# Optimization experiments

Hardware: AMD Instinct MI355X
Metric: run time of the kernel (lower is better)

Reference implementation:

```python
import jax, jax.numpy as jnp
import numpy as np

B, T, C, H = 4, 2048, 1024, 16
D = C // H  # head_dim = 64


def setup_inputs() -> dict:
    key = jax.random.key(0)
    k1, k2, k3 = jax.random.split(key, 3)
    x = jax.random.normal(k1, (B, T, C), dtype=jnp.float32)
    w_attn = jax.random.normal(k2, (C, 3 * C), dtype=jnp.float32) * (1.0 / np.sqrt(C))
    b_attn = jnp.zeros((3 * C,), dtype=jnp.float32)
    w_proj = jax.random.normal(k3, (C, C), dtype=jnp.float32) * (1.0 / np.sqrt(C))
    b_proj = jnp.zeros((C,), dtype=jnp.float32)
    return {"x": x, "w_attn": w_attn, "b_attn": b_attn, "w_proj": w_proj, "b_proj": b_proj}


def reference(x, w_attn, b_attn, w_proj, b_proj):
    Bx, Tx, Cx = x.shape
    qkv = x @ w_attn + b_attn                      # (B, T, 3C)
    q, k, v = jnp.split(qkv, 3, axis=2)
    # (B, T, C) -> (B, H, T, D)
    q = q.reshape(Bx, Tx, H, D).transpose(0, 2, 1, 3)
    k = k.reshape(Bx, Tx, H, D).transpose(0, 2, 1, 3)
    v = v.reshape(Bx, Tx, H, D).transpose(0, 2, 1, 3)
    scores = jnp.einsum('bhqd,bhkd->bhqk', q, k) / jnp.sqrt(jnp.float32(D))
    causal = jnp.tril(jnp.ones((Tx, Tx), dtype=bool))
    scores = jnp.where(causal[None, None], scores, jnp.float32(-jnp.inf))
    probs = jax.nn.softmax(scores, axis=-1)
    out = jnp.einsum('bhqk,bhkd->bhqd', probs, v)  # (B, H, T, D)
    out = out.transpose(0, 2, 1, 3).reshape(Bx, Tx, Cx)
    return out @ w_proj + b_proj
```

## Files before the change

kernel.cpp:

```cpp
#include <hip/hip_runtime.h>

#define AS1 __attribute__((address_space(1)))
#define AS3 __attribute__((address_space(3)))

using bf16x8  = __attribute__((ext_vector_type(8))) __bf16;
using floatx4 = __attribute__((ext_vector_type(4))) float;

#define SCQ 0.18033688f

__device__ inline ushort f2b(float f) {
    __bf16 h = (__bf16)f;
    return __builtin_bit_cast(ushort, h);
}

__global__ void k_conv(const float* __restrict__ in, ushort* __restrict__ out, int n) {
    int i = (blockIdx.x * 256 + threadIdx.x) * 4;
    if (i < n) {
        float4 v = *(const float4*)(in + i);
        ushort4 o;
        o.x = f2b(v.x); o.y = f2b(v.y); o.z = f2b(v.z); o.w = f2b(v.w);
        *(ushort4*)(out + i) = o;
    }
}

__global__ void k_transpose(const float* __restrict__ in, ushort* __restrict__ out,
                            int R, int Ncol, float scale, int scale_cols) {
    __shared__ float tile[32][33];
    int tx = threadIdx.x & 31, ty = threadIdx.x >> 5;
    int c0 = blockIdx.x * 32, r0 = blockIdx.y * 32;
    for (int i = 0; i < 32; i += 8)
        tile[ty + i][tx] = in[(size_t)(r0 + ty + i) * Ncol + c0 + tx];
    __syncthreads();
    for (int i = 0; i < 32; i += 8) {
        int n = c0 + ty + i;
        float v = tile[tx][ty + i];
        if (n < scale_cols) v *= scale;
        out[(size_t)n * R + r0 + tx] = f2b(v);
    }
}

__global__ __launch_bounds__(256, 2) void k_gemm_bt(
    const ushort* __restrict__ A, const ushort* __restrict__ Bt,
    const float* __restrict__ bias, float* __restrict__ outv,
    int M, int N, int K)
{
    __shared__ __align__(16) ushort As[128 * 32];
    __shared__ __align__(16) ushort Bs[128 * 32];
    int tid = threadIdx.x;
    int m0 = blockIdx.y * 128, n0 = blockIdx.x * 128;
    int lane = tid & 63;
    int wm = (tid >> 7) * 64;
    int wn = ((tid >> 6) & 1) * 64;
    int lr = lane & 15, quad = lane >> 4, lk = quad * 8;

    floatx4 acc[4][4] = {};
    const ushort* ag = A  + (size_t)(m0 + (tid >> 2)) * K + (tid & 3) * 8;
    const ushort* bg = Bt + (size_t)(n0 + (tid >> 2)) * K + (tid & 3) * 8;
    ushort* asd = &As[tid * 8];
    ushort* bsd = &Bs[tid * 8];

    for (int kt = 0; kt < K; kt += 32) {
        __builtin_amdgcn_global_load_lds((const AS1 unsigned int*)(ag + kt),                  (AS3 unsigned int*)(asd),        16, 0, 0);
        __builtin_amdgcn_global_load_lds((const AS1 unsigned int*)(ag + kt + (size_t)64 * K), (AS3 unsigned int*)(asd + 2048), 16, 0, 0);
        __builtin_amdgcn_global_load_lds((const AS1 unsigned int*)(bg + kt),                  (AS3 unsigned int*)(bsd),        16, 0, 0);
        __builtin_amdgcn_global_load_lds((const AS1 unsigned int*)(bg + kt + (size_t)64 * K), (AS3 unsigned int*)(bsd + 2048), 16, 0, 0);
        asm volatile("s_waitcnt vmcnt(0)" ::: "memory");
        __syncthreads();
        bf16x8 af[4], bf[4];
        #pragma unroll
        for (int i = 0; i < 4; ++i) af[i] = *(const bf16x8*)&As[(wm + 16 * i + lr) * 32 + lk];
        #pragma unroll
        for (int j = 0; j < 4; ++j) bf[j] = *(const bf16x8*)&Bs[(wn + 16 * j + lr) * 32 + lk];
        #pragma unroll
        for (int i = 0; i < 4; ++i)
            #pragma unroll
            for (int j = 0; j < 4; ++j)
                acc[i][j] = __builtin_amdgcn_mfma_f32_16x16x32_bf16(af[i], bf[j], acc[i][j], 0, 0, 0);
        __syncthreads();
    }

    #pragma unroll
    for (int j = 0; j < 4; ++j) {
        int col = n0 + wn + 16 * j + lr;
        float bv = bias[col];
        #pragma unroll
        for (int i = 0; i < 4; ++i) {
            int row = m0 + wm + 16 * i + quad * 4;
            #pragma unroll
            for (int r = 0; r < 4; ++r)
                outv[(size_t)(row + r) * N + col] = acc[i][j][r] + bv;
        }
    }
}

__global__ __launch_bounds__(256, 2) void k_gemm_qkv(
    const ushort* __restrict__ A, const ushort* __restrict__ Bt,
    const float* __restrict__ bias, ushort* __restrict__ qkv, ushort* __restrict__ vt)
{
    constexpr int K = 1024;
    __shared__ __align__(16) ushort As[128 * 32];
    __shared__ __align__(16) ushort Bs[128 * 32];
    int tid = threadIdx.x;
    int m0 = blockIdx.y * 128, n0 = blockIdx.x * 128;
    int lane = tid & 63;
    int wm = (tid >> 7) * 64;
    int wn = ((tid >> 6) & 1) * 64;
    int lr = lane & 15, quad = lane >> 4, lk = quad * 8;

    floatx4 acc[4][4] = {};
    const ushort* ag = A  + (size_t)(m0 + (tid >> 2)) * K + (tid & 3) * 8;
    const ushort* bg = Bt + (size_t)(n0 + (tid >> 2)) * K + (tid & 3) * 8;
    ushort* asd = &As[tid * 8];
    ushort* bsd = &Bs[tid * 8];

    for (int kt = 0; kt < K; kt += 32) {
        __builtin_amdgcn_global_load_lds((const AS1 unsigned int*)(ag + kt),                  (AS3 unsigned int*)(asd),        16, 0, 0);
        __builtin_amdgcn_global_load_lds((const AS1 unsigned int*)(ag + kt + (size_t)64 * K), (AS3 unsigned int*)(asd + 2048), 16, 0, 0);
        __builtin_amdgcn_global_load_lds((const AS1 unsigned int*)(bg + kt),                  (AS3 unsigned int*)(bsd),        16, 0, 0);
        __builtin_amdgcn_global_load_lds((const AS1 unsigned int*)(bg + kt + (size_t)64 * K), (AS3 unsigned int*)(bsd + 2048), 16, 0, 0);
        asm volatile("s_waitcnt vmcnt(0)" ::: "memory");
        __syncthreads();
        bf16x8 af[4], bf[4];
        #pragma unroll
        for (int i = 0; i < 4; ++i) af[i] = *(const bf16x8*)&As[(wm + 16 * i + lr) * 32 + lk];
        #pragma unroll
        for (int j = 0; j < 4; ++j) bf[j] = *(const bf16x8*)&Bs[(wn + 16 * j + lr) * 32 + lk];
        #pragma unroll
        for (int i = 0; i < 4; ++i)
            #pragma unroll
            for (int j = 0; j < 4; ++j)
                acc[i][j] = __builtin_amdgcn_mfma_f32_16x16x32_bf16(af[i], bf[j], acc[i][j], 0, 0, 0);
        __syncthreads();
    }

    int bb = m0 >> 11;
    #pragma unroll
    for (int j = 0; j < 4; ++j) {
        int col = n0 + wn + 16 * j + lr;
        float bv = bias[col];
        if (col < 1024) bv *= SCQ;
        if (col < 2048) {
            #pragma unroll
            for (int i = 0; i < 4; ++i) {
                int row = m0 + wm + 16 * i + quad * 4;
                #pragma unroll
                for (int r = 0; r < 4; ++r)
                    qkv[(size_t)(row + r) * 2048 + col] = f2b(acc[i][j][r] + bv);
            }
        } else {
            int h = (col - 2048) >> 6, d = (col - 2048) & 63;
            ushort* vbase = vt + ((size_t)(bb * 16 + h) * 64 + d) * 2048;
            #pragma unroll
            for (int i = 0; i < 4; ++i) {
                int t0 = (m0 + wm + 16 * i + quad * 4) & 2047;
                ushort4 pk;
                ((ushort*)&pk)[0] = f2b(acc[i][j][0] + bv);
                ((ushort*)&pk)[1] = f2b(acc[i][j][1] + bv);
                ((ushort*)&pk)[2] = f2b(acc[i][j][2] + bv);
                ((ushort*)&pk)[3] = f2b(acc[i][j][3] + bv);
                *(ushort4*)&vbase[t0] = pk;
            }
        }
    }
}

__global__ __launch_bounds__(512, 4) void k_attn(const ushort* __restrict__ qkv,
                                                 const ushort* __restrict__ vt,
                                                 ushort* __restrict__ out)
{
    constexpr int T = 2048, SQK = 2048, C = 1024;
    __shared__ __align__(16) ushort Ks[64 * 64];
    __shared__ __align__(16) ushort Vs[64 * 64];
    __shared__ __align__(16) ushort Ps[8 * 16 * 72];
    int tid = threadIdx.x;
    int lane = tid & 63, wave = tid >> 6;
    int lr = lane & 15, quad = lane >> 4, lk = quad * 8;
    int bh = blockIdx.y;
    int b = bh >> 4, h = bh & 15;
    size_t base = (size_t)b * T * SQK;
    const ushort* kg0 = qkv + base + 1024 + h * 64;
    const ushort* vg0 = vt + (size_t)bh * 64 * 2048;
    ushort* psw = &Ps[wave * 16 * 72];

    int srow = tid >> 3;
    int sg   = (tid & 7) ^ (srow & 7);
    ushort* ksdst = &Ks[tid * 8];
    ushort* vsdst = &Vs[tid * 8];
    const ushort* kgs = kg0 + (size_t)srow * SQK + sg * 8;
    const ushort* vgs = vg0 + (size_t)srow * 2048 + sg * 8;

    bf16x8 ones;
    #pragma unroll
    for (int i = 0; i < 8; ++i) ones[i] = (__bf16)1.0f;
    int c0 = (quad ^ (lr & 7)) * 8;
    int c1 = ((4 + quad) ^ (lr & 7)) * 8;

    int qts[2] = { (int)blockIdx.x, 15 - (int)blockIdx.x };
    for (int ti = 0; ti < 2; ++ti) {
        int qt = qts[ti];
        int qrow = qt * 128 + wave * 16;
        int kt_d = qrow >> 6;
        const ushort* qp = qkv + base + (size_t)(qrow + lr) * SQK + h * 64;
        bf16x8 aq0 = *(const bf16x8*)(qp + lk);
        bf16x8 aq1 = *(const bf16x8*)(qp + 32 + lk);
        floatx4 o[4] = {};
        floatx4 lacc = {};
        int ktmax = 2 * qt + 1;

        for (int kt = 0; kt <= ktmax; ++kt) {
            __syncthreads();
            __builtin_amdgcn_global_load_lds((const AS1 unsigned int*)(kgs + (size_t)kt * 64 * SQK),
                                             (AS3 unsigned int*)ksdst, 16, 0, 0);
            __builtin_amdgcn_global_load_lds((const AS1 unsigned int*)(vgs + kt * 64),
                                             (AS3 unsigned int*)vsdst, 16, 0, 0);
            asm volatile("s_waitcnt vmcnt(0)" ::: "memory");
            __syncthreads();
            if (kt > kt_d) continue;

            floatx4 s[4];
            #pragma unroll
            for (int j = 0; j < 4; ++j) {
                const ushort* kr = &Ks[(16 * j + lr) * 64];
                bf16x8 bk0 = *(const bf16x8*)(kr + c0);
                bf16x8 bk1 = *(const bf16x8*)(kr + c1);
                floatx4 z = {};
                s[j] = __builtin_amdgcn_mfma_f32_16x16x32_bf16(aq0, bk0, z, 0, 0, 0);
                s[j] = __builtin_amdgcn_mfma_f32_16x16x32_bf16(aq1, bk1, s[j], 0, 0, 0);
            }
            if (kt == kt_d) {
                int qg = qrow + quad * 4, kb = kt * 64;
                #pragma unroll
                for (int r = 0; r < 4; ++r)
                    #pragma unroll
                    for (int j = 0; j < 4; ++j) {
                        float p = ((kb + 16 * j + lr) > (qg + r)) ? 0.f : exp2f(s[j][r]);
                        psw[(quad * 4 + r) * 72 + 16 * j + lr] = f2b(p);
                    }
            } else {
                #pragma unroll
                for (int r = 0; r < 4; ++r)
                    #pragma unroll
                    for (int j = 0; j < 4; ++j)
                        psw[(quad * 4 + r) * 72 + 16 * j + lr] = f2b(exp2f(s[j][r]));
            }
            asm volatile("s_waitcnt lgkmcnt(0)" ::: "memory");
            bf16x8 ap0 = *(const bf16x8*)&psw[lr * 72 + lk];
            bf16x8 ap1 = *(const bf16x8*)&psw[lr * 72 + 32 + lk];
            lacc = __builtin_amdgcn_mfma_f32_16x16x32_bf16(ap0, ones, lacc, 0, 0, 0);
            lacc = __builtin_amdgcn_mfma_f32_16x16x32_bf16(ap1, ones, lacc, 0, 0, 0);
            #pragma unroll
            for (int jd = 0; jd < 4; ++jd) {
                const ushort* vr = &Vs[(16 * jd + lr) * 64];
                bf16x8 bv0 = *(const bf16x8*)(vr + c0);
                bf16x8 bv1 = *(const bf16x8*)(vr + c1);
                o[jd] = __builtin_amdgcn_mfma_f32_16x16x32_bf16(ap0, bv0, o[jd], 0, 0, 0);
                o[jd] = __builtin_amdgcn_mfma_f32_16x16x32_bf16(ap1, bv1, o[jd], 0, 0, 0);
            }
        }

        #pragma unroll
        for (int r = 0; r < 4; ++r) {
            float inv = 1.0f / lacc[r];
            int row = b * T + qrow + quad * 4 + r;
            #pragma unroll
            for (int jd = 0; jd < 4; ++jd)
                out[(size_t)row * C + h * 64 + 16 * jd + lr] = f2b(o[jd][r] * inv);
        }
    }
}

extern "C" void kernel_launch(void* const* d_in, const int* in_sizes, int n_in,
                              void* d_out, int out_size, void* d_ws, size_t ws_size,
                              hipStream_t stream) {
    const float* x      = (const float*)d_in[0];
    const float* w_attn = (const float*)d_in[1];
    const float* b_attn = (const float*)d_in[2];
    const float* w_proj = (const float*)d_in[3];
    const float* b_proj = (const float*)d_in[4];
    float* out = (float*)d_out;

    constexpr int Bb = 4, T = 2048, C = 1024;
    constexpr int M = Bb * T;

    ushort* xb  = (ushort*)d_ws;
    ushort* waT = xb  + (size_t)M * C;
    ushort* wpT = waT + (size_t)3 * C * C;
    ushort* qkv = wpT + (size_t)C * C;
    ushort* vt  = qkv + (size_t)M * 2 * C;
    ushort* ao  = vt  + (size_t)64 * 64 * T;

    k_conv<<<(M * C / 4 + 255) / 256, 256, 0, stream>>>(x, xb, M * C);
    k_transpose<<<dim3(3 * C / 32, C / 32), 256, 0, stream>>>(w_attn, waT, C, 3 * C, SCQ, C);
    k_transpose<<<dim3(C / 32, C / 32), 256, 0, stream>>>(w_proj, wpT, C, C, 1.0f, 0);
    k_gemm_qkv<<<dim3(3 * C / 128, M / 128), 256, 0, stream>>>(xb, waT, b_attn, qkv, vt);
    k_attn<<<dim3(8, Bb * 16), 512, 0, stream>>>(qkv, vt, ao);
    k_gemm_bt<<<dim3(C / 128, M / 128), 256, 0, stream>>>(ao, wpT, b_proj, out, M, C, C);
}
```

Before: 262.5 us.

## Restructure attention to 128-key tiles with 32 query rows per wave

The attention kernel moves from 512 threads handling 16 query rows per wave over 64-key tiles to 256 threads handling 32 query rows per wave over 128-key tiles. S is computed transposed (K as the A operand) so each lane writes packed 4-wide P values, and each V fragment is reused across two query subtiles. The aim is to halve the number of K/V loads and barriers per query block, raise MFMA reuse per LDS read, and drop the idle iterations of the old loop. The cost is more registers, more shared memory per block and fewer waves per block.

```diff
diff --git a/kernel.cpp b/kernel.cpp
--- a/kernel.cpp
+++ b/kernel.cpp
@@ -164,108 +164,138 @@
     }
 }
 
-__global__ __launch_bounds__(512, 4) void k_attn(const ushort* __restrict__ qkv,
+__global__ __launch_bounds__(256, 2) void k_attn(const ushort* __restrict__ qkv,
                                                  const ushort* __restrict__ vt,
                                                  ushort* __restrict__ out)
 {
     constexpr int T = 2048, SQK = 2048, C = 1024;
-    __shared__ __align__(16) ushort Ks[64 * 64];
-    __shared__ __align__(16) ushort Vs[64 * 64];
-    __shared__ __align__(16) ushort Ps[8 * 16 * 72];
+    constexpr int PSTR = 136;
+    __shared__ __align__(16) ushort Ks[128 * 64];
+    __shared__ __align__(16) ushort Vs[64 * 128];
+    __shared__ __align__(16) ushort Ps[4 * 32 * PSTR];
     int tid = threadIdx.x;
     int lane = tid & 63, wave = tid >> 6;
-    int lr = lane & 15, quad = lane >> 4, lk = quad * 8;
+    int lr = lane & 15, quad = lane >> 4;
     int bh = blockIdx.y;
     int b = bh >> 4, h = bh & 15;
     size_t base = (size_t)b * T * SQK;
     const ushort* kg0 = qkv + base + 1024 + h * 64;
     const ushort* vg0 = vt + (size_t)bh * 64 * 2048;
-    ushort* psw = &Ps[wave * 16 * 72];
-
-    int srow = tid >> 3;
-    int sg   = (tid & 7) ^ (srow & 7);
-    ushort* ksdst = &Ks[tid * 8];
-    ushort* vsdst = &Vs[tid * 8];
-    const ushort* kgs = kg0 + (size_t)srow * SQK + sg * 8;
-    const ushort* vgs = vg0 + (size_t)srow * 2048 + sg * 8;
+    ushort* psw = &Ps[wave * 32 * PSTR];
 
     bf16x8 ones;
     #pragma unroll
     for (int i = 0; i < 8; ++i) ones[i] = (__bf16)1.0f;
-    int c0 = (quad ^ (lr & 7)) * 8;
-    int c1 = ((4 + quad) ^ (lr & 7)) * 8;
+
+    int kslot[4], vslot[4];
+    #pragma unroll
+    for (int it = 0; it < 4; ++it) { kslot[it] = tid + 256 * it; vslot[it] = tid + 256 * it; }
 
     int qts[2] = { (int)blockIdx.x, 15 - (int)blockIdx.x };
     for (int ti = 0; ti < 2; ++ti) {
         int qt = qts[ti];
-        int qrow = qt * 128 + wave * 16;
-        int kt_d = qrow >> 6;
-        const ushort* qp = qkv + base + (size_t)(qrow + lr) * SQK + h * 64;
-        bf16x8 aq0 = *(const bf16x8*)(qp + lk);
-        bf16x8 aq1 = *(const bf16x8*)(qp + 32 + lk);
-        floatx4 o[4] = {};
-        floatx4 lacc = {};
-        int ktmax = 2 * qt + 1;
-
-        for (int kt = 0; kt <= ktmax; ++kt) {
+        int qrowW = qt * 128 + wave * 32;
+        const ushort* qp0 = qkv + base + (size_t)(qrowW + lr) * SQK + h * 64;
+        const ushort* qp1 = qkv + base + (size_t)(qrowW + 16 + lr) * SQK + h * 64;
+        bf16x8 aq00 = *(const bf16x8*)(qp0 + quad * 8);
+        bf16x8 aq01 = *(const bf16x8*)(qp0 + 32 + quad * 8);
+        bf16x8 aq10 = *(const bf16x8*)(qp1 + quad * 8);
+        bf16x8 aq11 = *(const bf16x8*)(qp1 + 32 + quad * 8);
+        floatx4 o[2][4] = {};
+        floatx4 lacc[2] = {};
+
+        for (int kt = 0; kt <= qt; ++kt) {
             __syncthreads();
-            __builtin_amdgcn_global_load_lds((const AS1 unsigned int*)(kgs + (size_t)kt * 64 * SQK),
-                                             (AS3 unsigned int*)ksdst, 16, 0, 0);
-            __builtin_amdgcn_global_load_lds((const AS1 unsigned int*)(vgs + kt * 64),
-                                             (AS3 unsigned int*)vsdst, 16, 0, 0);
+            #pragma unroll
+            for (int it = 0; it < 4; ++it) {
+                int sl = kslot[it];
+                int key = sl >> 3, g = (sl & 7) ^ (key & 7);
+                __builtin_amdgcn_global_load_lds(
+                    (const AS1 unsigned int*)(kg0 + (size_t)(kt * 128 + key) * SQK + g * 8),
+                    (AS3 unsigned int*)&Ks[sl * 8], 16, 0, 0);
+            }
+            #pragma unroll
+            for (int it = 0; it < 4; ++it) {
+                int sl = vslot[it];
+                int dim = sl >> 4, g = (sl & 15) ^ (dim & 15);
+                __builtin_amdgcn_global_load_lds(
+                    (const AS1 unsigned int*)(vg0 + (size_t)dim * 2048 + kt * 128 + g * 8),
+                    (AS3 unsigned int*)&Vs[sl * 8], 16, 0, 0);
+            }
             asm volatile("s_waitcnt vmcnt(0)" ::: "memory");
             __syncthreads();
-            if (kt > kt_d) continue;
-
-            floatx4 s[4];
-            #pragma unroll
-            for (int j = 0; j < 4; ++j) {
-                const ushort* kr = &Ks[(16 * j + lr) * 64];
-                bf16x8 bk0 = *(const bf16x8*)(kr + c0);
-                bf16x8 bk1 = *(const bf16x8*)(kr + c1);
+
+            bool diag = (kt == qt);
+            #pragma unroll
+            for (int jk = 0; jk < 8; ++jk) {
+                const ushort* kr = &Ks[(16 * jk + lr) * 64];
+                bf16x8 ak0 = *(const bf16x8*)(kr + ((quad) ^ (lr & 7)) * 8);
+                bf16x8 ak1 = *(const bf16x8*)(kr + ((4 + quad) ^ (lr & 7)) * 8);
                 floatx4 z = {};
-                s[j] = __builtin_amdgcn_mfma_f32_16x16x32_bf16(aq0, bk0, z, 0, 0, 0);
-                s[j] = __builtin_amdgcn_mfma_f32_16x16x32_bf16(aq1, bk1, s[j], 0, 0, 0);
-            }
-            if (kt == kt_d) {
-                int qg = qrow + quad * 4, kb = kt * 64;
+                floatx4 st0 = __builtin_amdgcn_mfma_f32_16x16x32_bf16(ak0, aq00, z, 0, 0, 0);
+                st0 = __builtin_amdgcn_mfma_f32_16x16x32_bf16(ak1, aq01, st0, 0, 0, 0);
+                floatx4 st1 = __builtin_amdgcn_mfma_f32_16x16x32_bf16(ak0, aq10, z, 0, 0, 0);
+                st1 = __builtin_amdgcn_mfma_f32_16x16x32_bf16(ak1, aq11, st1, 0, 0, 0);
+                int kloc = 16 * jk + quad * 4;
+                if (diag) {
+                    int q0l = wave * 32 + lr;
+                    float p00 = (kloc + 0 > q0l) ? 0.f : exp2f(st0[0]);
+                    float p01 = (kloc + 1 > q0l) ? 0.f : exp2f(st0[1]);
+                    float p02 = (kloc + 2 > q0l) ? 0.f : exp2f(st0[2]);
+                    float p03 = (kloc + 3 > q0l) ? 0.f : exp2f(st0[3]);
+                    int q1l = q0l + 16;
+                    float p10 = (kloc + 0 > q1l) ? 0.f : exp2f(st1[0]);
+                    float p11 = (kloc + 1 > q1l) ? 0.f : exp2f(st1[1]);
+                    float p12 = (kloc + 2 > q1l) ? 0.f : exp2f(st1[2]);
+                    float p13 = (kloc + 3 > q1l) ? 0.f : exp2f(st1[3]);
+                    uint2 w0, w1;
+                    w0.x = (unsigned)f2b(p00) | ((unsigned)f2b(p01) << 16);
+                    w0.y = (unsigned)f2b(p02) | ((unsigned)f2b(p03) << 16);
+                    w1.x = (unsigned)f2b(p10) | ((unsigned)f2b(p11) << 16);
+                    w1.y = (unsigned)f2b(p12) | ((unsigned)f2b(p13) << 16);
+                    *(uint2*)&psw[(lr) * PSTR + kloc]      = w0;
+                    *(uint2*)&psw[(16 + lr) * PSTR + kloc] = w1;
+                } else {
+                    uint2 w0, w1;
+                    w0.x = (unsigned)f2b(exp2f(st0[0])) | ((unsigned)f2b(exp2f(st0[1])) << 16);
+                    w0.y = (unsigned)f2b(exp2f(st0[2])) | ((unsigned)f2b(exp2f(st0[3])) << 16);
+                    w1.x = (unsigned)f2b(exp2f(st1[0])) | ((unsigned)f2b(exp2f(st1[1])) << 16);
+                    w1.y = (unsigned)f2b(exp2f(st1[2])) | ((unsigned)f2b(exp2f(st1[3])) << 16);
+                    *(uint2*)&psw[(lr) * PSTR + kloc]      = w0;
+                    *(uint2*)&psw[(16 + lr) * PSTR + kloc] = w1;
+                }
+            }
+            asm volatile("s_waitcnt lgkmcnt(0)" ::: "memory");
+            bf16x8 ap[2][4];
+            #pragma unroll
+            for (int t = 0; t < 2; ++t)
                 #pragma unroll
-                for (int r = 0; r < 4; ++r)
-                    #pragma unroll
-                    for (int j = 0; j < 4; ++j) {
-                        float p = ((kb + 16 * j + lr) > (qg + r)) ? 0.f : exp2f(s[j][r]);
-                        psw[(quad * 4 + r) * 72 + 16 * j + lr] = f2b(p);
-                    }
-            } else {
+                for (int s = 0; s < 4; ++s) {
+                    ap[t][s] = *(const bf16x8*)&psw[(t * 16 + lr) * PSTR + s * 32 + quad * 8];
+                    lacc[t] = __builtin_amdgcn_mfma_f32_16x16x32_bf16(ap[t][s], ones, lacc[t], 0, 0, 0);
+                }
+            #pragma unroll
+            for (int jd = 0; jd < 4; ++jd) {
+                const ushort* vr = &Vs[(16 * jd + lr) * 128];
                 #pragma unroll
-                for (int r = 0; r < 4; ++r)
-                    #pragma unroll
-                    for (int j = 0; j < 4; ++j)
-                        psw[(quad * 4 + r) * 72 + 16 * j + lr] = f2b(exp2f(s[j][r]));
-            }
-            asm volatile("s_waitcnt lgkmcnt(0)" ::: "memory");
-            bf16x8 ap0 = *(const bf16x8*)&psw[lr * 72 + lk];
-            bf16x8 ap1 = *(const bf16x8*)&psw[lr * 72 + 32 + lk];
-            lacc = __builtin_amdgcn_mfma_f32_16x16x32_bf16(ap0, ones, lacc, 0, 0, 0);
-            lacc = __builtin_amdgcn_mfma_f32_16x16x32_bf16(ap1, ones, lacc, 0, 0, 0);
-            #pragma unroll
-            for (int jd = 0; jd < 4; ++jd) {
-                const ushort* vr = &Vs[(16 * jd + lr) * 64];
-                bf16x8 bv0 = *(const bf16x8*)(vr + c0);
-                bf16x8 bv1 = *(const bf16x8*)(vr + c1);
-                o[jd] = __builtin_amdgcn_mfma_f32_16x16x32_bf16(ap0, bv0, o[jd], 0, 0, 0);
-                o[jd] = __builtin_amdgcn_mfma_f32_16x16x32_bf16(ap1, bv1, o[jd], 0, 0, 0);
+                for (int s = 0; s < 4; ++s) {
+                    bf16x8 bv = *(const bf16x8*)(vr + ((4 * s + quad) ^ lr) * 8);
+                    o[0][jd] = __builtin_amdgcn_mfma_f32_16x16x32_bf16(ap[0][s], bv, o[0][jd], 0, 0, 0);
+                    o[1][jd] = __builtin_amdgcn_mfma_f32_16x16x32_bf16(ap[1][s], bv, o[1][jd], 0, 0, 0);
+                }
             }
         }
 
         #pragma unroll
-        for (int r = 0; r < 4; ++r) {
-            float inv = 1.0f / lacc[r];
-            int row = b * T + qrow + quad * 4 + r;
-            #pragma unroll
-            for (int jd = 0; jd < 4; ++jd)
-                out[(size_t)row * C + h * 64 + 16 * jd + lr] = f2b(o[jd][r] * inv);
-        }
+        for (int t = 0; t < 2; ++t)
+            #pragma unroll
+            for (int r = 0; r < 4; ++r) {
+                float inv = 1.0f / lacc[t][r];
+                int row = b * T + qrowW + t * 16 + quad * 4 + r;
+                #pragma unroll
+                for (int jd = 0; jd < 4; ++jd)
+                    out[(size_t)row * C + h * 64 + 16 * jd + lr] = f2b(o[t][jd][r] * inv);
+            }
     }
 }
 
@@ -293,6 +323,6 @@
     k_transpose<<<dim3(3 * C / 32, C / 32), 256, 0, stream>>>(w_attn, waT, C, 3 * C, SCQ, C);
     k_transpose<<<dim3(C / 32, C / 32), 256, 0, stream>>>(w_proj, wpT, C, C, 1.0f, 0);
     k_gemm_qkv<<<dim3(3 * C / 128, M / 128), 256, 0, stream>>>(xb, waT, b_attn, qkv, vt);
-    k_attn<<<dim3(8, Bb * 16), 512, 0, stream>>>(qkv, vt, ao);
+    k_attn<<<dim3(8, Bb * 16), 256, 0, stream>>>(qkv, vt, ao);
     k_gemm_bt<<<dim3(C / 128, M / 128), 256, 0, stream>>>(ao, wpT, b_proj, out, M, C, C);
 }
```

New measurement: 285.0 us. +8.6%, slower.

## Double-buffer K/V tiles in LDS and compute transposed S for packed P stores

Applied to the files above, without the earlier changes.

The K and V shared-memory tiles are doubled so the next tile's global-to-LDS load is issued right after the barrier and overlaps the current tile's QK^T, softmax and PV work. This replaces the load-then-wait-every-iteration pattern. S is also computed as K·Q^T, so each lane holds four consecutive keys for one query and writes P as a single packed 8-byte store instead of sixteen scalar stores. The cost is twice the LDS for K and V, which may reduce occupancy at 512 threads per block.

```diff
diff --git a/kernel.cpp b/kernel.cpp
--- a/kernel.cpp
+++ b/kernel.cpp
@@ -169,8 +169,8 @@
                                                  ushort* __restrict__ out)
 {
     constexpr int T = 2048, SQK = 2048, C = 1024;
-    __shared__ __align__(16) ushort Ks[64 * 64];
-    __shared__ __align__(16) ushort Vs[64 * 64];
+    __shared__ __align__(16) ushort Ks[2 * 64 * 64];
+    __shared__ __align__(16) ushort Vs[2 * 64 * 64];
     __shared__ __align__(16) ushort Ps[8 * 16 * 72];
     int tid = threadIdx.x;
     int lane = tid & 63, wave = tid >> 6;
@@ -184,8 +184,6 @@
 
     int srow = tid >> 3;
     int sg   = (tid & 7) ^ (srow & 7);
-    ushort* ksdst = &Ks[tid * 8];
-    ushort* vsdst = &Vs[tid * 8];
     const ushort* kgs = kg0 + (size_t)srow * SQK + sg * 8;
     const ushort* vgs = vg0 + (size_t)srow * 2048 + sg * 8;
 
@@ -200,6 +198,7 @@
         int qt = qts[ti];
         int qrow = qt * 128 + wave * 16;
         int kt_d = qrow >> 6;
+        int qoff = (qrow & 63) + lr;
         const ushort* qp = qkv + base + (size_t)(qrow + lr) * SQK + h * 64;
         bf16x8 aq0 = *(const bf16x8*)(qp + lk);
         bf16x8 aq1 = *(const bf16x8*)(qp + 32 + lk);
@@ -207,41 +206,52 @@
         floatx4 lacc = {};
         int ktmax = 2 * qt + 1;
 
+        __syncthreads();
+        __builtin_amdgcn_global_load_lds((const AS1 unsigned int*)(kgs),
+                                         (AS3 unsigned int*)&Ks[tid * 8], 16, 0, 0);
+        __builtin_amdgcn_global_load_lds((const AS1 unsigned int*)(vgs),
+                                         (AS3 unsigned int*)&Vs[tid * 8], 16, 0, 0);
+
         for (int kt = 0; kt <= ktmax; ++kt) {
-            __syncthreads();
-            __builtin_amdgcn_global_load_lds((const AS1 unsigned int*)(kgs + (size_t)kt * 64 * SQK),
-                                             (AS3 unsigned int*)ksdst, 16, 0, 0);
-            __builtin_amdgcn_global_load_lds((const AS1 unsigned int*)(vgs + kt * 64),
-                                             (AS3 unsigned int*)vsdst, 16, 0, 0);
+            int cur = kt & 1;
             asm volatile("s_waitcnt vmcnt(0)" ::: "memory");
             __syncthreads();
+            if (kt < ktmax) {
+                int nb = cur ^ 1;
+                __builtin_amdgcn_global_load_lds(
+                    (const AS1 unsigned int*)(kgs + (size_t)(kt + 1) * 64 * SQK),
+                    (AS3 unsigned int*)&Ks[nb * 4096 + tid * 8], 16, 0, 0);
+                __builtin_amdgcn_global_load_lds(
+                    (const AS1 unsigned int*)(vgs + (kt + 1) * 64),
+                    (AS3 unsigned int*)&Vs[nb * 4096 + tid * 8], 16, 0, 0);
+            }
             if (kt > kt_d) continue;
-
-            floatx4 s[4];
-            #pragma unroll
-            for (int j = 0; j < 4; ++j) {
-                const ushort* kr = &Ks[(16 * j + lr) * 64];
-                bf16x8 bk0 = *(const bf16x8*)(kr + c0);
-                bf16x8 bk1 = *(const bf16x8*)(kr + c1);
+            const ushort* Kb = &Ks[cur * 4096];
+            const ushort* Vb = &Vs[cur * 4096];
+            bool diag = (kt == kt_d);
+
+            #pragma unroll
+            for (int jk = 0; jk < 4; ++jk) {
+                const ushort* kr = &Kb[(16 * jk + lr) * 64];
+                bf16x8 ak0 = *(const bf16x8*)(kr + c0);
+                bf16x8 ak1 = *(const bf16x8*)(kr + c1);
                 floatx4 z = {};
-                s[j] = __builtin_amdgcn_mfma_f32_16x16x32_bf16(aq0, bk0, z, 0, 0, 0);
-                s[j] = __builtin_amdgcn_mfma_f32_16x16x32_bf16(aq1, bk1, s[j], 0, 0, 0);
-            }
-            if (kt == kt_d) {
-                int qg = qrow + quad * 4, kb = kt * 64;
-                #pragma unroll
-                for (int r = 0; r < 4; ++r)
-                    #pragma unroll
-                    for (int j = 0; j < 4; ++j) {
-                        float p = ((kb + 16 * j + lr) > (qg + r)) ? 0.f : exp2f(s[j][r]);
-                        psw[(quad * 4 + r) * 72 + 16 * j + lr] = f2b(p);
-                    }
-            } else {
-                #pragma unroll
-                for (int r = 0; r < 4; ++r)
-                    #pragma unroll
-                    for (int j = 0; j < 4; ++j)
-                        psw[(quad * 4 + r) * 72 + 16 * j + lr] = f2b(exp2f(s[j][r]));
+                floatx4 st = __builtin_amdgcn_mfma_f32_16x16x32_bf16(ak0, aq0, z, 0, 0, 0);
+                st = __builtin_amdgcn_mfma_f32_16x16x32_bf16(ak1, aq1, st, 0, 0, 0);
+                int kloc = 16 * jk + quad * 4;
+                uint2 w;
+                if (diag) {
+                    float p0 = (kloc + 0 > qoff) ? 0.f : exp2f(st[0]);
+                    float p1 = (kloc + 1 > qoff) ? 0.f : exp2f(st[1]);
+                    float p2 = (kloc + 2 > qoff) ? 0.f : exp2f(st[2]);
+                    float p3 = (kloc + 3 > qoff) ? 0.f : exp2f(st[3]);
+                    w.x = (unsigned)f2b(p0) | ((unsigned)f2b(p1) << 16);
+                    w.y = (unsigned)f2b(p2) | ((unsigned)f2b(p3) << 16);
+                } else {
+                    w.x = (unsigned)f2b(exp2f(st[0])) | ((unsigned)f2b(exp2f(st[1])) << 16);
+                    w.y = (unsigned)f2b(exp2f(st[2])) | ((unsigned)f2b(exp2f(st[3])) << 16);
+                }
+                *(uint2*)&psw[lr * 72 + kloc] = w;
             }
             asm volatile("s_waitcnt lgkmcnt(0)" ::: "memory");
             bf16x8 ap0 = *(const bf16x8*)&psw[lr * 72 + lk];
@@ -250,7 +260,7 @@
             lacc = __builtin_amdgcn_mfma_f32_16x16x32_bf16(ap1, ones, lacc, 0, 0, 0);
             #pragma unroll
             for (int jd = 0; jd < 4; ++jd) {
-                const ushort* vr = &Vs[(16 * jd + lr) * 64];
+                const ushort* vr = &Vb[(16 * jd + lr) * 64];
                 bf16x8 bv0 = *(const bf16x8*)(vr + c0);
                 bf16x8 bv1 = *(const bf16x8*)(vr + c1);
                 o[jd] = __builtin_amdgcn_mfma_f32_16x16x32_bf16(ap0, bv0, o[jd], 0, 0, 0);
```

New measurement: 267.7 us. +2.0%, slower.

## Merge prep kernels into one launch and double GEMM K-tile to 64

Applied to the files above, without the earlier changes.

Folds the x bf16 conversion and both weight transposes into a single k_prep launch that dispatches on block index, removing two kernel launches. Both GEMM kernels now stage a 128x64 K-slice per iteration instead of 128x32, halving the number of barrier and waitcnt round trips and issuing two MFMAs per accumulator per step. LDS use per block doubles to 32KB. The new 64-element row stride may add LDS bank conflicts on the fragment reads.

```diff
diff --git a/kernel.cpp b/kernel.cpp
--- a/kernel.cpp
+++ b/kernel.cpp
@@ -13,21 +13,32 @@
     return __builtin_bit_cast(ushort, h);
 }
 
-__global__ void k_conv(const float* __restrict__ in, ushort* __restrict__ out, int n) {
-    int i = (blockIdx.x * 256 + threadIdx.x) * 4;
-    if (i < n) {
-        float4 v = *(const float4*)(in + i);
+__global__ void k_prep(const float* __restrict__ x, ushort* __restrict__ xb,
+                       const float* __restrict__ wa, ushort* __restrict__ waT,
+                       const float* __restrict__ wp, ushort* __restrict__ wpT)
+{
+    __shared__ float tile[32][33];
+    int blk = blockIdx.x;
+    if (blk < 8192) {
+        int i = (blk * 256 + threadIdx.x) * 4;
+        float4 v = *(const float4*)(x + i);
         ushort4 o;
         o.x = f2b(v.x); o.y = f2b(v.y); o.z = f2b(v.z); o.w = f2b(v.w);
-        *(ushort4*)(out + i) = o;
-    }
-}
-
-__global__ void k_transpose(const float* __restrict__ in, ushort* __restrict__ out,
-                            int R, int Ncol, float scale, int scale_cols) {
-    __shared__ float tile[32][33];
+        *(ushort4*)(xb + i) = o;
+        return;
+    }
+    const float* in; ushort* out; int R, Ncol, bx, by; float scale; int scale_cols;
+    if (blk < 11264) {
+        int idx = blk - 8192;
+        in = wa; out = waT; R = 1024; Ncol = 3072;
+        bx = idx % 96; by = idx / 96; scale = SCQ; scale_cols = 1024;
+    } else {
+        int idx = blk - 11264;
+        in = wp; out = wpT; R = 1024; Ncol = 1024;
+        bx = idx % 32; by = idx / 32; scale = 1.0f; scale_cols = 0;
+    }
     int tx = threadIdx.x & 31, ty = threadIdx.x >> 5;
-    int c0 = blockIdx.x * 32, r0 = blockIdx.y * 32;
+    int c0 = bx * 32, r0 = by * 32;
     for (int i = 0; i < 32; i += 8)
         tile[ty + i][tx] = in[(size_t)(r0 + ty + i) * Ncol + c0 + tx];
     __syncthreads();
@@ -44,38 +55,54 @@
     const float* __restrict__ bias, float* __restrict__ outv,
     int M, int N, int K)
 {
-    __shared__ __align__(16) ushort As[128 * 32];
-    __shared__ __align__(16) ushort Bs[128 * 32];
+    __shared__ __align__(16) ushort As[128 * 64];
+    __shared__ __align__(16) ushort Bs[128 * 64];
     int tid = threadIdx.x;
     int m0 = blockIdx.y * 128, n0 = blockIdx.x * 128;
     int lane = tid & 63;
     int wm = (tid >> 7) * 64;
     int wn = ((tid >> 6) & 1) * 64;
-    int lr = lane & 15, quad = lane >> 4, lk = quad * 8;
+    int lr = lane & 15, quad = lane >> 4;
 
     floatx4 acc[4][4] = {};
-    const ushort* ag = A  + (size_t)(m0 + (tid >> 2)) * K + (tid & 3) * 8;
-    const ushort* bg = Bt + (size_t)(n0 + (tid >> 2)) * K + (tid & 3) * 8;
-    ushort* asd = &As[tid * 8];
-    ushort* bsd = &Bs[tid * 8];
-
-    for (int kt = 0; kt < K; kt += 32) {
-        __builtin_amdgcn_global_load_lds((const AS1 unsigned int*)(ag + kt),                  (AS3 unsigned int*)(asd),        16, 0, 0);
-        __builtin_amdgcn_global_load_lds((const AS1 unsigned int*)(ag + kt + (size_t)64 * K), (AS3 unsigned int*)(asd + 2048), 16, 0, 0);
-        __builtin_amdgcn_global_load_lds((const AS1 unsigned int*)(bg + kt),                  (AS3 unsigned int*)(bsd),        16, 0, 0);
-        __builtin_amdgcn_global_load_lds((const AS1 unsigned int*)(bg + kt + (size_t)64 * K), (AS3 unsigned int*)(bsd + 2048), 16, 0, 0);
+    const ushort* ags[4]; const ushort* bgs[4]; int sdst[4];
+    #pragma unroll
+    for (int it = 0; it < 4; ++it) {
+        int slot = tid + 256 * it;
+        int row = slot >> 3, ch = slot & 7;
+        ags[it] = A  + (size_t)(m0 + row) * K + ch * 8;
+        bgs[it] = Bt + (size_t)(n0 + row) * K + ch * 8;
+        sdst[it] = slot * 8;
+    }
+
+    for (int kt = 0; kt < K; kt += 64) {
+        #pragma unroll
+        for (int it = 0; it < 4; ++it) {
+            __builtin_amdgcn_global_load_lds((const AS1 unsigned int*)(ags[it] + kt),
+                                             (AS3 unsigned int*)&As[sdst[it]], 16, 0, 0);
+            __builtin_amdgcn_global_load_lds((const AS1 unsigned int*)(bgs[it] + kt),
+                                             (AS3 unsigned int*)&Bs[sdst[it]], 16, 0, 0);
+        }
         asm volatile("s_waitcnt vmcnt(0)" ::: "memory");
         __syncthreads();
-        bf16x8 af[4], bf[4];
-        #pragma unroll
-        for (int i = 0; i < 4; ++i) af[i] = *(const bf16x8*)&As[(wm + 16 * i + lr) * 32 + lk];
-        #pragma unroll
-        for (int j = 0; j < 4; ++j) bf[j] = *(const bf16x8*)&Bs[(wn + 16 * j + lr) * 32 + lk];
+        bf16x8 af[4][2], bf[4][2];
+        #pragma unroll
+        for (int i = 0; i < 4; ++i) {
+            af[i][0] = *(const bf16x8*)&As[(wm + 16 * i + lr) * 64 + quad * 8];
+            af[i][1] = *(const bf16x8*)&As[(wm + 16 * i + lr) * 64 + 32 + quad * 8];
+        }
+        #pragma unroll
+        for (int j = 0; j < 4; ++j) {
+            bf[j][0] = *(const bf16x8*)&Bs[(wn + 16 * j + lr) * 64 + quad * 8];
+            bf[j][1] = *(const bf16x8*)&Bs[(wn + 16 * j + lr) * 64 + 32 + quad * 8];
+        }
         #pragma unroll
         for (int i = 0; i < 4; ++i)
             #pragma unroll
-            for (int j = 0; j < 4; ++j)
-                acc[i][j] = __builtin_amdgcn_mfma_f32_16x16x32_bf16(af[i], bf[j], acc[i][j], 0, 0, 0);
+            for (int j = 0; j < 4; ++j) {
+                acc[i][j] = __builtin_amdgcn_mfma_f32_16x16x32_bf16(af[i][0], bf[j][0], acc[i][j], 0, 0, 0);
+                acc[i][j] = __builtin_amdgcn_mfma_f32_16x16x32_bf16(af[i][1], bf[j][1], acc[i][j], 0, 0, 0);
+            }
         __syncthreads();
     }
 
@@ -98,38 +125,54 @@
     const float* __restrict__ bias, ushort* __restrict__ qkv, ushort* __restrict__ vt)
 {
     constexpr int K = 1024;
-    __shared__ __align__(16) ushort As[128 * 32];
-    __shared__ __align__(16) ushort Bs[128 * 32];
+    __shared__ __align__(16) ushort As[128 * 64];
+    __shared__ __align__(16) ushort Bs[128 * 64];
     int tid = threadIdx.x;
     int m0 = blockIdx.y * 128, n0 = blockIdx.x * 128;
     int lane = tid & 63;
     int wm = (tid >> 7) * 64;
     int wn = ((tid >> 6) & 1) * 64;
-    int lr = lane & 15, quad = lane >> 4, lk = quad * 8;
+    int lr = lane & 15, quad = lane >> 4;
 
     floatx4 acc[4][4] = {};
-    const ushort* ag = A  + (size_t)(m0 + (tid >> 2)) * K + (tid & 3) * 8;
-    const ushort* bg = Bt + (size_t)(n0 + (tid >> 2)) * K + (tid & 3) * 8;
-    ushort* asd = &As[tid * 8];
-    ushort* bsd = &Bs[tid * 8];
-
-    for (int kt = 0; kt < K; kt += 32) {
-        __builtin_amdgcn_global_load_lds((const AS1 unsigned int*)(ag + kt),                  (AS3 unsigned int*)(asd),        16, 0, 0);
-        __builtin_amdgcn_global_load_lds((const AS1 unsigned int*)(ag + kt + (size_t)64 * K), (AS3 unsigned int*)(asd + 2048), 16, 0, 0);
-        __builtin_amdgcn_global_load_lds((const AS1 unsigned int*)(bg + kt),                  (AS3 unsigned int*)(bsd),        16, 0, 0);
-        __builtin_amdgcn_global_load_lds((const AS1 unsigned int*)(bg + kt + (size_t)64 * K), (AS3 unsigned int*)(bsd + 2048), 16, 0, 0);
+    const ushort* ags[4]; const ushort* bgs[4]; int sdst[4];
+    #pragma unroll
+    for (int it = 0; it < 4; ++it) {
+        int slot = tid + 256 * it;
+        int row = slot >> 3, ch = slot & 7;
+        ags[it] = A  + (size_t)(m0 + row) * K + ch * 8;
+        bgs[it] = Bt + (size_t)(n0 + row) * K + ch * 8;
+        sdst[it] = slot * 8;
+    }
+
+    for (int kt = 0; kt < K; kt += 64) {
+        #pragma unroll
+        for (int it = 0; it < 4; ++it) {
+            __builtin_amdgcn_global_load_lds((const AS1 unsigned int*)(ags[it] + kt),
+                                             (AS3 unsigned int*)&As[sdst[it]], 16, 0, 0);
+            __builtin_amdgcn_global_load_lds((const AS1 unsigned int*)(bgs[it] + kt),
+                                             (AS3 unsigned int*)&Bs[sdst[it]], 16, 0, 0);
+        }
         asm volatile("s_waitcnt vmcnt(0)" ::: "memory");
         __syncthreads();
-        bf16x8 af[4], bf[4];
-        #pragma unroll
-        for (int i = 0; i < 4; ++i) af[i] = *(const bf16x8*)&As[(wm + 16 * i + lr) * 32 + lk];
-        #pragma unroll
-        for (int j = 0; j < 4; ++j) bf[j] = *(const bf16x8*)&Bs[(wn + 16 * j + lr) * 32 + lk];
+        bf16x8 af[4][2], bf[4][2];
+        #pragma unroll
+        for (int i = 0; i < 4; ++i) {
+            af[i][0] = *(const bf16x8*)&As[(wm + 16 * i + lr) * 64 + quad * 8];
+            af[i][1] = *(const bf16x8*)&As[(wm + 16 * i + lr) * 64 + 32 + quad * 8];
+        }
+        #pragma unroll
+        for (int j = 0; j < 4; ++j) {
+            bf[j][0] = *(const bf16x8*)&Bs[(wn + 16 * j + lr) * 64 + quad * 8];
+            bf[j][1] = *(const bf16x8*)&Bs[(wn + 16 * j + lr) * 64 + 32 + quad * 8];
+        }
         #pragma unroll
         for (int i = 0; i < 4; ++i)
             #pragma unroll
-            for (int j = 0; j < 4; ++j)
-                acc[i][j] = __builtin_amdgcn_mfma_f32_16x16x32_bf16(af[i], bf[j], acc[i][j], 0, 0, 0);
+            for (int j = 0; j < 4; ++j) {
+                acc[i][j] = __builtin_amdgcn_mfma_f32_16x16x32_bf16(af[i][0], bf[j][0], acc[i][j], 0, 0, 0);
+                acc[i][j] = __builtin_amdgcn_mfma_f32_16x16x32_bf16(af[i][1], bf[j][1], acc[i][j], 0, 0, 0);
+            }
         __syncthreads();
     }
 
@@ -289,9 +332,7 @@
     ushort* vt  = qkv + (size_t)M * 2 * C;
     ushort* ao  = vt  + (size_t)64 * 64 * T;
 
-    k_conv<<<(M * C / 4 + 255) / 256, 256, 0, stream>>>(x, xb, M * C);
-    k_transpose<<<dim3(3 * C / 32, C / 32), 256, 0, stream>>>(w_attn, waT, C, 3 * C, SCQ, C);
-    k_transpose<<<dim3(C / 32, C / 32), 256, 0, stream>>>(w_proj, wpT, C, C, 1.0f, 0);
+    k_prep<<<12288, 256, 0, stream>>>(x, xb, w_attn, waT, w_proj, wpT);
     k_gemm_qkv<<<dim3(3 * C / 128, M / 128), 256, 0, stream>>>(xb, waT, b_attn, qkv, vt);
     k_attn<<<dim3(8, Bb * 16), 512, 0, stream>>>(qkv, vt, ao);
     k_gemm_bt<<<dim3(C / 128, M / 128), 256, 0, stream>>>(ao, wpT, b_proj, out, M, C, C);
```

Result: faster. 256.4 us (-2.3%).
